# Performance work log

Hardware: AMD Instinct MI355X
Metric: run time of the kernel (lower is better)

The kernel has to match this reference:

```python
import jax, jax.numpy as jnp
import numpy as np

B, T, E, H, HD, L, V = 4, 1024, 1024, 16, 64, 8, 32000
FF = 4 * E
SCALE = E ** -0.5  # NOTE: original scales by embed_size**-0.5, not head_size**-0.5
EPS = 1e-5


def setup_inputs() -> dict:
    key = jax.random.key(0)
    ks = jax.random.split(key, 22)
    s = 0.02
    n = lambda k, shape: (jax.random.normal(k, shape) * s).astype(jnp.float32)
    return {
        "x": jax.random.randint(ks[0], (B, T), 0, V),
        "tok_emb": n(ks[1], (V, E)),
        "pos_emb": n(ks[2], (T, E)),
        "Wq": n(ks[3], (L, H, E, HD)),
        "Wk": n(ks[4], (L, H, E, HD)),
        "Wv": n(ks[5], (L, H, E, HD)),
        "Wproj": n(ks[6], (L, E, E)),
        "bproj": jnp.zeros((L, E), jnp.float32),
        "ln1g": jnp.ones((L, E), jnp.float32),
        "ln1b": jnp.zeros((L, E), jnp.float32),
        "ln2g": jnp.ones((L, E), jnp.float32),
        "ln2b": jnp.zeros((L, E), jnp.float32),
        "W1": n(ks[7], (L, E, FF)),
        "b1": jnp.zeros((L, FF), jnp.float32),
        "W2": n(ks[8], (L, FF, E)),
        "b2": jnp.zeros((L, E), jnp.float32),
        "lnfg": jnp.ones((E,), jnp.float32),
        "lnfb": jnp.zeros((E,), jnp.float32),
        "Wout": n(ks[9], (E, V)),
        "bout": jnp.zeros((V,), jnp.float32),
    }


def _ln(x, g, b):
    m = jnp.mean(x, axis=-1, keepdims=True)
    v = jnp.mean(jnp.square(x - m), axis=-1, keepdims=True)
    return (x - m) * jax.lax.rsqrt(v + EPS) * g + b


def _gpt(x, tok_emb, pos_emb, Wq, Wk, Wv, Wproj, bproj, ln1g, ln1b, ln2g, ln2b,
         W1, b1, W2, b2, lnfg, lnfb, Wout, bout):
    h = tok_emb[x] + pos_emb[None, :, :]  # [B,T,E]
    mask = jnp.tril(jnp.ones((T, T), bool))  # causal

    def block(h, p):
        wq, wk, wv, wp, bp, g1, bb1n, g2, bb2n, w1, bb1, w2, bb2 = p
        xn = _ln(h, g1, bb1n)
        q = jnp.einsum('bte,hed->bhtd', xn, wq)
        k = jnp.einsum('bte,hed->bhtd', xn, wk)
        v = jnp.einsum('bte,hed->bhtd', xn, wv)
        scores = jnp.einsum('bhtd,bhsd->bhts', q, k) * SCALE
        scores = jnp.where(mask, scores, -jnp.inf)
        w = jax.nn.softmax(scores, axis=-1)
        a = jnp.einsum('bhts,bhsd->bhtd', w, v)  # [B,H,T,HD]
        a = a.transpose(0, 2, 1, 3).reshape(B, T, E)  # concat heads
        h = h + jnp.einsum('bte,ef->btf', a, wp) + bp
        xn2 = _ln(h, g2, bb2n)
        ff = jax.nn.gelu(jnp.einsum('bte,ef->btf', xn2, w1) + bb1, approximate=False)
        h = h + jnp.einsum('btf,fe->bte', ff, w2) + bb2
        return h, None

    params = (Wq, Wk, Wv, Wproj, bproj, ln1g, ln1b, ln2g, ln2b, W1, b1, W2, b2)
    h, _ = jax.lax.scan(block, h, params)
    h = _ln(h, lnfg, lnfb)
    return jnp.einsum('bte,ev->btv', h, Wout) + bout  # logits [B,T,V]


def reference(x, tok_emb, pos_emb, Wq, Wk, Wv, Wproj, bproj, ln1g, ln1b, ln2g,
              ln2b, W1, b1, W2, b2, lnfg, lnfb, Wout, bout):
    return _gpt(x, tok_emb, pos_emb, Wq, Wk, Wv, Wproj, bproj, ln1g, ln1b,
                ln2g, ln2b, W1, b1, W2, b2, lnfg, lnfb, Wout, bout)
```

## Files before the change

kernel.cpp:

```cpp
#include <hip/hip_runtime.h>

#define B_ 4
#define T_ 1024
#define E_ 1024
#define H_ 16
#define HD_ 64
#define L_ 8
#define V_ 32000
#define FF_ 4096
#define M_ (B_*T_)

typedef unsigned short u16;
typedef __attribute__((ext_vector_type(8))) short bf16x8;
typedef __attribute__((ext_vector_type(4))) float f32x4;

#define AS1V(p) ((__attribute__((address_space(1))) void*)(p))
#define AS3V(p) ((__attribute__((address_space(3))) void*)(p))
#define XSW(row) (((row) & 7) << 4)

#define GBAR  asm volatile("s_barrier" ::: "memory")
#define WVM8  asm volatile("s_waitcnt vmcnt(8)" ::: "memory")
#define WVM0  asm volatile("s_waitcnt vmcnt(0)" ::: "memory")

__device__ __forceinline__ u16 f2bf(float f) {
    unsigned int u = __float_as_uint(f);
    u += 0x7FFFu + ((u >> 16) & 1u);
    return (u16)(u >> 16);
}
__device__ __forceinline__ float bf2f(u16 v) {
    return __uint_as_float(((unsigned int)v) << 16);
}
__device__ __forceinline__ float ldf(const float* p, long i) { return p[i]; }
__device__ __forceinline__ float ldf(const u16*   p, long i) { return bf2f(p[i]); }

__device__ __forceinline__ int xcd_swz(int orig, int nwg) {
    int q8 = nwg >> 3, r8 = nwg & 7;
    int xcd = orig & 7, sub = orig >> 3;
    return (xcd < r8 ? xcd*(q8+1) : r8*(q8+1) + (xcd-r8)*q8) + sub;
}

template<typename ST>
__global__ void k_transpose(const ST* __restrict__ src, u16* __restrict__ dst,
                            int K, int N, long srs, long drs,
                            int ZH, long szb, long szh, long dzb, long dzh)
{
    __shared__ float tile[32][33];
    int z = blockIdx.z; int zb = z / ZH, zh = z % ZH;
    const ST* s = src + (long)zb*szb + (long)zh*szh;
    u16* d = dst + (long)zb*dzb + (long)zh*dzh;
    int k0 = blockIdx.y * 32, n0 = blockIdx.x * 32;
    int tx = threadIdx.x, ty = threadIdx.y;
    for (int i = ty; i < 32; i += 8) {
        int k = k0 + i, n = n0 + tx;
        tile[i][tx] = (k < K && n < N) ? ldf(s, (long)k*srs + n) : 0.f;
    }
    __syncthreads();
    for (int i = ty; i < 32; i += 8) {
        int n = n0 + i, k = k0 + tx;
        if (n < N && k < K) d[(long)n*drs + k] = f2bf(tile[tx][i]);
    }
}

__global__ void k_embed(const int* __restrict__ x, const float* __restrict__ tok,
                        const float* __restrict__ pos, float* __restrict__ h)
{
    long i = (long)blockIdx.x * 256 + threadIdx.x;
    int e4 = (int)(i & (E_/4 - 1));
    long bt = i >> 8;
    int t = (int)(bt & (T_ - 1));
    int id = x[bt];
    float4 a = *(const float4*)(tok + (long)id*E_ + e4*4);
    float4 p = *(const float4*)(pos + (long)t*E_ + e4*4);
    float4 o; o.x=a.x+p.x; o.y=a.y+p.y; o.z=a.z+p.z; o.w=a.w+p.w;
    *(float4*)(h + bt*E_ + e4*4) = o;
}

__global__ void k_ln(const float* __restrict__ in, const float* __restrict__ g,
                     const float* __restrict__ b, u16* __restrict__ out)
{
    int row = blockIdx.x, tid = threadIdx.x;
    float4 v = *(const float4*)(in + (long)row*E_ + tid*4);
    float s = v.x + v.y + v.z + v.w;
    float ss = v.x*v.x + v.y*v.y + v.z*v.z + v.w*v.w;
    #pragma unroll
    for (int o = 32; o; o >>= 1) { s += __shfl_down(s, o); ss += __shfl_down(ss, o); }
    __shared__ float r0[4], r1[4];
    if ((tid & 63) == 0) { r0[tid >> 6] = s; r1[tid >> 6] = ss; }
    __syncthreads();
    s  = r0[0] + r0[1] + r0[2] + r0[3];
    ss = r1[0] + r1[1] + r1[2] + r1[3];
    float mean = s * (1.f/E_);
    float rstd = rsqrtf(ss * (1.f/E_) - mean*mean + 1e-5f);
    float4 gv = *(const float4*)(g + tid*4);
    float4 bv = *(const float4*)(b + tid*4);
    ushort4 pk;
    pk.x = f2bf((v.x - mean)*rstd*gv.x + bv.x);
    pk.y = f2bf((v.y - mean)*rstd*gv.y + bv.y);
    pk.z = f2bf((v.z - mean)*rstd*gv.z + bv.z);
    pk.w = f2bf((v.w - mean)*rstd*gv.w + bv.w);
    *(ushort4*)(out + (long)row*E_ + tid*4) = pk;
}

__global__ __launch_bounds__(256, 2)
void k_flash(const u16* __restrict__ qkv, const u16* __restrict__ vt,
             u16* __restrict__ attno)
{
    __shared__ alignas(16) char lds[65536];
    const int wg = xcd_swz(blockIdx.x, gridDim.x);
    const int bh = wg >> 3, qt = 7 - (wg & 7);
    const int b = bh >> 4, hh = bh & 15;

    const int tid = threadIdx.x, w = tid >> 6, lane = tid & 63;
    const int fr = lane & 15, sel = lane >> 4;
    const int xs = XSW(fr);

    const char* qb = (const char*)(qkv + (long)b*T_*3*E_ + (size_t)hh*HD_);
    const char* kb = (const char*)(qkv + (long)b*T_*3*E_ + E_ + (size_t)hh*HD_);
    const char* vb = (const char*)(vt + (size_t)bh*HD_*T_);
    const int q0 = qt << 7;

    bf16x8 qa[2][2];
    #pragma unroll
    for (int rf = 0; rf < 2; ++rf)
        #pragma unroll
        for (int t = 0; t < 2; ++t) {
            int row = q0 + w*32 + rf*16 + fr;
            qa[rf][t] = *(const bf16x8*)(qb + (long)row*(3*E_*2) + t*64 + sel*16);
        }

    f32x4 oacc[2][4];
    float mrow[2][4], lrow[2][4];
    #pragma unroll
    for (int rf = 0; rf < 2; ++rf) {
        #pragma unroll
        for (int cf = 0; cf < 4; ++cf) oacc[rf][cf] = (f32x4){0.f,0.f,0.f,0.f};
        #pragma unroll
        for (int r = 0; r < 4; ++r) { mrow[rf][r] = -1e30f; lrow[rf][r] = 0.f; }
    }

    char* Ks  = lds;
    char* Vts = lds + 16384;
    char* Pw  = lds + 32768 + w*8192;

    for (int kv = 0; kv <= qt; ++kv) {
        const int s0 = kv << 7;
        __syncthreads();
        #pragma unroll
        for (int c = 0; c < 4; ++c) {
            int o = c*4096 + tid*16;
            int row = o >> 7;
            int offl = (o & 127) ^ XSW(row);
            const char* ga = kb + (long)(s0 + row)*(3*E_*2) + offl;
            __builtin_amdgcn_global_load_lds(AS1V(ga), AS3V(Ks + c*4096 + (tid >> 6)*1024), 16, 0, 0);
        }
        #pragma unroll
        for (int c = 0; c < 4; ++c) {
            int o = c*4096 + tid*16;
            int row = o >> 8;
            int offl = (o & 255) ^ XSW(row);
            const char* ga = vb + (long)row*(T_*2) + s0*2 + offl;
            __builtin_amdgcn_global_load_lds(AS1V(ga), AS3V(Vts + c*4096 + (tid >> 6)*1024), 16, 0, 0);
        }
        __syncthreads();

        f32x4 sacc[2][8];
        #pragma unroll
        for (int rf = 0; rf < 2; ++rf)
            #pragma unroll
            for (int cf = 0; cf < 8; ++cf) sacc[rf][cf] = (f32x4){0.f,0.f,0.f,0.f};
        __builtin_amdgcn_s_setprio(1);
        #pragma unroll
        for (int t = 0; t < 2; ++t) {
            bf16x8 kf[8];
            #pragma unroll
            for (int cf = 0; cf < 8; ++cf) {
                int srow = cf*16 + fr;
                kf[cf] = *(const bf16x8*)(Ks + srow*128 + ((t*64 + sel*16) ^ xs));
            }
            #pragma unroll
            for (int rf = 0; rf < 2; ++rf)
                #pragma unroll
                for (int cf = 0; cf < 8; ++cf)
                    sacc[rf][cf] = __builtin_amdgcn_mfma_f32_16x16x32_bf16(
                        qa[rf][t], kf[cf], sacc[rf][cf], 0, 0, 0);
        }
        __builtin_amdgcn_s_setprio(0);

        const bool diag = (kv == qt);
        #pragma unroll
        for (int rf = 0; rf < 2; ++rf)
            #pragma unroll
            for (int r = 0; r < 4; ++r) {
                int rowg = q0 + w*32 + rf*16 + sel*4 + r;
                float mx = -1e30f;
                #pragma unroll
                for (int cf = 0; cf < 8; ++cf) {
                    float v = sacc[rf][cf][r] * 0.03125f;
                    if (diag && (s0 + cf*16 + fr) > rowg) v = -1e30f;
                    sacc[rf][cf][r] = v;
                    mx = fmaxf(mx, v);
                }
                #pragma unroll
                for (int o = 1; o < 16; o <<= 1) mx = fmaxf(mx, __shfl_xor(mx, o));
                float mold = mrow[rf][r];
                float mnew = fmaxf(mold, mx);
                float alpha = __expf(mold - mnew);
                float sum = 0.f;
                #pragma unroll
                for (int cf = 0; cf < 8; ++cf) {
                    float p = __expf(sacc[rf][cf][r] - mnew);
                    sacc[rf][cf][r] = p;
                    sum += p;
                }
                #pragma unroll
                for (int o = 1; o < 16; o <<= 1) sum += __shfl_xor(sum, o);
                mrow[rf][r] = mnew;
                lrow[rf][r] = lrow[rf][r]*alpha + sum;
                #pragma unroll
                for (int cf = 0; cf < 4; ++cf) oacc[rf][cf][r] *= alpha;
            }

        #pragma unroll
        for (int rf = 0; rf < 2; ++rf)
            #pragma unroll
            for (int r = 0; r < 4; ++r) {
                int rl = rf*16 + sel*4 + r;
                char* base = Pw + rl*256;
                int sw = XSW(rl);
                #pragma unroll
                for (int cf = 0; cf < 8; ++cf)
                    *(u16*)(base + ((cf*32 + fr*2) ^ sw)) = f2bf(sacc[rf][cf][r]);
            }

        __builtin_amdgcn_s_setprio(1);
        #pragma unroll
        for (int ts = 0; ts < 4; ++ts) {
            bf16x8 pa[2], vf[4];
            #pragma unroll
            for (int rf = 0; rf < 2; ++rf)
                pa[rf] = *(const bf16x8*)(Pw + (rf*16 + fr)*256 + ((ts*64 + sel*16) ^ xs));
            #pragma unroll
            for (int cf = 0; cf < 4; ++cf)
                vf[cf] = *(const bf16x8*)(Vts + (cf*16 + fr)*256 + ((ts*64 + sel*16) ^ xs));
            #pragma unroll
            for (int rf = 0; rf < 2; ++rf)
                #pragma unroll
                for (int cf = 0; cf < 4; ++cf)
                    oacc[rf][cf] = __builtin_amdgcn_mfma_f32_16x16x32_bf16(
                        pa[rf], vf[cf], oacc[rf][cf], 0, 0, 0);
        }
        __builtin_amdgcn_s_setprio(0);
    }

    u16* ab = attno + ((long)b*T_ + q0 + w*32)*E_ + (size_t)hh*HD_;
    #pragma unroll
    for (int rf = 0; rf < 2; ++rf)
        #pragma unroll
        for (int r = 0; r < 4; ++r) {
            float rinv = 1.f / lrow[rf][r];
            int rl = rf*16 + sel*4 + r;
            #pragma unroll
            for (int cf = 0; cf < 4; ++cf)
                ab[(long)rl*E_ + cf*16 + fr] = f2bf(oacc[rf][cf][r] * rinv);
        }
}

__global__ __launch_bounds__(256, 2)
void k_gemm128(const u16* __restrict__ A, const u16* __restrict__ Bt,
               float* __restrict__ C, const float* __restrict__ bias,
               const float* __restrict__ res,
               long lda, long ldb, long ldc, int Kk, int nTN)
{
    __shared__ alignas(128) char lds[65536];
    const int wg = xcd_swz(blockIdx.x, gridDim.x);
    const int m0 = (wg / nTN) << 7, n0 = (wg % nTN) << 7;

    const int tid = threadIdx.x, wid = tid >> 6, lane = tid & 63;
    const int fr = lane & 15, sel = lane >> 4;
    const int wr = wid >> 1, wc = wid & 1;
    const int xs = XSW(fr);
    const int KT = Kk >> 6;

    const long lda2 = lda*2, ldb2 = ldb*2;
    const int rowL = tid >> 3;
    const int offl = (((tid & 7) ^ (rowL & 7)) << 4);
    const char* pA = (const char*)A + ((long)(m0 + rowL))*lda2 + offl;
    const char* pB = (const char*)Bt + ((long)(n0 + rowL))*ldb2 + offl;
    char* ldwA = lds + (wid << 10);
    char* ldwB = lds + 32768 + (wid << 10);

    auto stageA = [&](int kt) {
        const int d = (kt & 1) << 14;
        const long kb = (long)kt << 7;
        #pragma unroll
        for (int c = 0; c < 4; ++c)
            __builtin_amdgcn_global_load_lds(AS1V(pA + (long)(c << 5)*lda2 + kb),
                                             AS3V(ldwA + d + (c << 12)), 16, 0, 0);
    };
    auto stageB = [&](int kt) {
        const int d = (kt & 1) << 14;
        const long kb = (long)kt << 7;
        #pragma unroll
        for (int c = 0; c < 4; ++c)
            __builtin_amdgcn_global_load_lds(AS1V(pB + (long)(c << 5)*ldb2 + kb),
                                             AS3V(ldwB + d + (c << 12)), 16, 0, 0);
    };

    f32x4 acc[4][4];
    #pragma unroll
    for (int i = 0; i < 4; ++i)
        #pragma unroll
        for (int j = 0; j < 4; ++j) acc[i][j] = (f32x4){0.f,0.f,0.f,0.f};

    stageA(0); stageB(0); stageA(1); stageB(1);
    WVM8; GBAR;

    for (int t = 0; t < KT; ++t) {
        const int d = (t & 1) << 14;
        bf16x8 a[4][2], b[4][2];
        #pragma unroll
        for (int m = 0; m < 4; ++m)
            #pragma unroll
            for (int tt = 0; tt < 2; ++tt)
                a[m][tt] = *(const bf16x8*)(lds + d +
                    (((wr*64 + m*16 + fr) << 7) + ((sel*16 + tt*64) ^ xs)));
        #pragma unroll
        for (int n = 0; n < 4; ++n)
            #pragma unroll
            for (int tt = 0; tt < 2; ++tt)
                b[n][tt] = *(const bf16x8*)(lds + 32768 + d +
                    (((wc*64 + n*16 + fr) << 7) + ((sel*16 + tt*64) ^ xs)));
        __builtin_amdgcn_s_setprio(1);
        #pragma unroll
        for (int m = 0; m < 4; ++m)
            #pragma unroll
            for (int n = 0; n < 4; ++n)
                #pragma unroll
                for (int tt = 0; tt < 2; ++tt)
                    acc[m][n] = __builtin_amdgcn_mfma_f32_16x16x32_bf16(
                        a[m][tt], b[n][tt], acc[m][n], 0, 0, 0);
        __builtin_amdgcn_s_setprio(0);
        GBAR;
        if (t + 2 < KT) {
            stageA(t+2); stageB(t+2);
            WVM8;
        } else {
            WVM0;
        }
        GBAR;
    }

    #pragma unroll
    for (int m = 0; m < 4; ++m) {
        #pragma unroll
        for (int rr = 0; rr < 4; ++rr) {
            const int row = m0 + wr*64 + m*16 + sel*4 + rr;
            #pragma unroll
            for (int n = 0; n < 4; ++n) {
                const int col = n0 + wc*64 + n*16 + fr;
                long idx = (long)row*ldc + col;
                C[idx] = acc[m][n][rr] + bias[col] + res[idx];
            }
        }
    }
}

template<int MODE>
__global__ __launch_bounds__(512, 2)
void k_gemm256(const u16* __restrict__ A, const u16* __restrict__ Bt,
               void* __restrict__ Cv, const float* __restrict__ bias,
               long lda, long ldb, long ldc, int Kk, int nTN)
{
    __shared__ alignas(128) char lds[131072];
    const int wg = xcd_swz(blockIdx.x, gridDim.x);
    const int m0 = (wg / nTN) << 8, n0 = (wg % nTN) << 8;

    const int tid = threadIdx.x, wid = tid >> 6, lane = tid & 63;
    const int fr = lane & 15, sel = lane >> 4;
    const int wr = wid >> 2, wc = wid & 3;
    const int xs = XSW(fr);
    const int KT = Kk >> 6;

    const long lda2 = lda*2, ldb2 = ldb*2;
    const int rowL = tid >> 3;
    const int offl = (((tid & 7) ^ (rowL & 7)) << 4);
    const char* pA = (const char*)A + ((long)(m0 + rowL))*lda2 + offl;
    const char* pB = (const char*)Bt + ((long)(n0 + rowL))*ldb2 + offl;
    char* ldwA = lds + (wid << 10);
    char* ldwB = lds + 65536 + (wid << 10);

    auto stageA = [&](int kt) {
        const int d = (kt & 1) << 15;
        const long kb = (long)kt << 7;
        #pragma unroll
        for (int hq = 0; hq < 4; ++hq)
            __builtin_amdgcn_global_load_lds(AS1V(pA + (long)(hq << 6)*lda2 + kb),
                                             AS3V(ldwA + d + (hq << 13)), 16, 0, 0);
    };
    auto stageB = [&](int kt) {
        const int d = (kt & 1) << 15;
        const long kb = (long)kt << 7;
        #pragma unroll
        for (int hq = 0; hq < 4; ++hq)
            __builtin_amdgcn_global_load_lds(AS1V(pB + (long)(hq << 6)*ldb2 + kb),
                                             AS3V(ldwB + d + (hq << 13)), 16, 0, 0);
    };

    bf16x8 a[4][2], b[2][2][2];
    f32x4 acc[8][4];
    #pragma unroll
    for (int i = 0; i < 8; ++i)
        #pragma unroll
        for (int j = 0; j < 4; ++j) acc[i][j] = (f32x4){0.f,0.f,0.f,0.f};

    auto readA = [&](int d, int rh) {
        const int base = (d << 15) + ((wr*128 + rh*64 + fr) << 7) + (sel << 4);
        #pragma unroll
        for (int rf = 0; rf < 4; ++rf)
            #pragma unroll
            for (int t = 0; t < 2; ++t)
                a[rf][t] = *(const bf16x8*)(lds + ((base + (rf << 11) + (t << 6)) ^ xs));
    };
    auto readB = [&](int d, int ch) {
        const int base = 65536 + (d << 15) + ((wc*64 + ch*32 + fr) << 7) + (sel << 4);
        #pragma unroll
        for (int cf = 0; cf < 2; ++cf)
            #pragma unroll
            for (int t = 0; t < 2; ++t)
                b[ch][cf][t] = *(const bf16x8*)(lds + ((base + (cf << 11) + (t << 6)) ^ xs));
    };
    auto mfma16 = [&](int rh, int ch) {
        __builtin_amdgcn_s_setprio(1);
        #pragma unroll
        for (int rf = 0; rf < 4; ++rf)
            #pragma unroll
            for (int cf = 0; cf < 2; ++cf)
                #pragma unroll
                for (int t = 0; t < 2; ++t)
                    acc[rh*4+rf][ch*2+cf] = __builtin_amdgcn_mfma_f32_16x16x32_bf16(
                        a[rf][t], b[ch][cf][t], acc[rh*4+rf][ch*2+cf], 0, 0, 0);
        __builtin_amdgcn_s_setprio(0);
    };

    stageA(0); stageB(0); stageA(1); stageB(1);
    WVM8; GBAR;

    for (int kt = 0; kt < KT; kt += 2) {
        const bool pf = (kt + 2) < KT;
        readA(0,0); readB(0,0);
        GBAR; mfma16(0,0); GBAR;
        readB(0,1);
        GBAR; mfma16(0,1); GBAR;
        readA(0,1); if (pf) stageB(kt+2);
        GBAR; mfma16(1,1); GBAR;
        if (pf) stageA(kt+2);
        GBAR; mfma16(1,0);
        if (pf) { WVM8; } else { WVM0; }
        GBAR;
        readA(1,0); readB(1,0);
        GBAR; mfma16(0,0); GBAR;
        readB(1,1);
        GBAR; mfma16(0,1); GBAR;
        readA(1,1); if (pf) stageB(kt+3);
        GBAR; mfma16(1,1); GBAR;
        if (pf) stageA(kt+3);
        GBAR; mfma16(1,0);
        if (pf) { WVM8; }
        GBAR;
    }

    #pragma unroll
    for (int rf = 0; rf < 8; ++rf) {
        const int row0 = m0 + wr*128 + rf*16 + (sel << 2);
        #pragma unroll
        for (int rr = 0; rr < 4; ++rr) {
            const long rbase = (long)(row0 + rr) * ldc;
            #pragma unroll
            for (int cf = 0; cf < 4; ++cf) {
                const int col = n0 + wc*64 + cf*16 + fr;
                float v = acc[rf][cf][rr];
                if constexpr (MODE == 0) {
                    ((u16*)Cv)[rbase + col] = f2bf(v);
                } else if constexpr (MODE == 2) {
                    float tt = v + bias[col];
                    ((u16*)Cv)[rbase + col] = f2bf(tt * 0.5f * (1.f + erff(tt * 0.70710678118f)));
                } else {
                    ((float*)Cv)[rbase + col] = v + bias[col];
                }
            }
        }
    }
}

extern "C" void kernel_launch(void* const* d_in, const int* in_sizes, int n_in,
                              void* d_out, int out_size, void* d_ws, size_t ws_size,
                              hipStream_t stream)
{
    (void)in_sizes; (void)n_in; (void)out_size; (void)ws_size;
    const int*   x   = (const int*)  d_in[0];
    const float* tok = (const float*)d_in[1];
    const float* pos = (const float*)d_in[2];
    const float* Wq  = (const float*)d_in[3];
    const float* Wk  = (const float*)d_in[4];
    const float* Wv  = (const float*)d_in[5];
    const float* Wp  = (const float*)d_in[6];
    const float* bp  = (const float*)d_in[7];
    const float* g1  = (const float*)d_in[8];
    const float* bb1 = (const float*)d_in[9];
    const float* g2  = (const float*)d_in[10];
    const float* bb2 = (const float*)d_in[11];
    const float* W1  = (const float*)d_in[12];
    const float* b1  = (const float*)d_in[13];
    const float* W2  = (const float*)d_in[14];
    const float* b2  = (const float*)d_in[15];
    const float* gF  = (const float*)d_in[16];
    const float* bF  = (const float*)d_in[17];
    const float* Wo  = (const float*)d_in[18];
    const float* bo  = (const float*)d_in[19];
    float* out = (float*)d_out;

    char* wsp = (char*)d_ws;
    auto alloc = [&](size_t bytes) { char* p = wsp; wsp += (bytes + 255) & ~(size_t)255; return p; };
    u16* WqkvT  = (u16*)alloc((size_t)L_*3*E_*E_*2);
    u16* WprojT = (u16*)alloc((size_t)L_*E_*E_*2);
    u16* W1T    = (u16*)alloc((size_t)L_*FF_*E_*2);
    u16* W2T    = (u16*)alloc((size_t)L_*E_*FF_*2);
    u16* WoutT  = (u16*)alloc((size_t)V_*E_*2);
    float* h    = (float*)alloc((size_t)M_*E_*4);
    u16* xn     = (u16*)alloc((size_t)M_*E_*2);
    u16* qkv    = (u16*)alloc((size_t)M_*3*E_*2);
    u16* vt     = (u16*)alloc((size_t)B_*H_*HD_*T_*2);
    u16* attno  = (u16*)alloc((size_t)M_*E_*2);
    u16* ffb    = (u16*)alloc((size_t)M_*FF_*2);

    dim3 tb(32, 8);
    k_transpose<float><<<dim3(HD_/32, E_/32, L_*H_), tb, 0, stream>>>(
        Wq, WqkvT, E_, HD_, (long)HD_, (long)E_,
        H_, (long)H_*E_*HD_, (long)E_*HD_, (long)3*E_*E_, (long)HD_*E_);
    k_transpose<float><<<dim3(HD_/32, E_/32, L_*H_), tb, 0, stream>>>(
        Wk, WqkvT + (size_t)E_*E_, E_, HD_, (long)HD_, (long)E_,
        H_, (long)H_*E_*HD_, (long)E_*HD_, (long)3*E_*E_, (long)HD_*E_);
    k_transpose<float><<<dim3(HD_/32, E_/32, L_*H_), tb, 0, stream>>>(
        Wv, WqkvT + (size_t)2*E_*E_, E_, HD_, (long)HD_, (long)E_,
        H_, (long)H_*E_*HD_, (long)E_*HD_, (long)3*E_*E_, (long)HD_*E_);
    k_transpose<float><<<dim3(E_/32, E_/32, L_), tb, 0, stream>>>(
        Wp, WprojT, E_, E_, (long)E_, (long)E_, 1, (long)E_*E_, 0, (long)E_*E_, 0);
    k_transpose<float><<<dim3(FF_/32, E_/32, L_), tb, 0, stream>>>(
        W1, W1T, E_, FF_, (long)FF_, (long)E_, 1, (long)E_*FF_, 0, (long)FF_*E_, 0);
    k_transpose<float><<<dim3(E_/32, FF_/32, L_), tb, 0, stream>>>(
        W2, W2T, FF_, E_, (long)E_, (long)FF_, 1, (long)FF_*E_, 0, (long)E_*FF_, 0);
    k_transpose<float><<<dim3(V_/32, E_/32, 1), tb, 0, stream>>>(
        Wo, WoutT, E_, V_, (long)V_, (long)E_, 1, 0, 0, 0, 0);
    k_embed<<<dim3(M_*E_/4/256), dim3(256), 0, stream>>>(x, tok, pos, h);

    auto gemm256 = [&](int mode, const u16* A, const u16* Bt, void* C, const float* bias,
                       int Mm, int Nn, int Kk, long lda, long ldb, long ldc) {
        int nTN = Nn >> 8;
        dim3 g((Mm >> 8) * nTN), blk(512);
        switch (mode) {
        case 0: k_gemm256<0><<<g, blk, 0, stream>>>(A, Bt, C, bias, lda, ldb, ldc, Kk, nTN); break;
        case 2: k_gemm256<2><<<g, blk, 0, stream>>>(A, Bt, C, bias, lda, ldb, ldc, Kk, nTN); break;
        case 4: k_gemm256<4><<<g, blk, 0, stream>>>(A, Bt, C, bias, lda, ldb, ldc, Kk, nTN); break;
        }
    };

    for (int l = 0; l < L_; ++l) {
        k_ln<<<dim3(M_), dim3(256), 0, stream>>>(h, g1 + (size_t)l*E_, bb1 + (size_t)l*E_, xn);
        gemm256(0, xn, WqkvT + (size_t)l*3*E_*E_, qkv, nullptr,
                M_, 3*E_, E_, (long)E_, (long)E_, (long)3*E_);
        k_transpose<u16><<<dim3(HD_/32, T_/32, B_*H_), tb, 0, stream>>>(
            qkv + 2*E_, vt, T_, HD_, (long)3*E_, (long)T_,
            H_, (long)T_*3*E_, (long)HD_, (long)H_*HD_*T_, (long)HD_*T_);
        k_flash<<<dim3(B_*H_*8), dim3(256), 0, stream>>>(qkv, vt, attno);
        k_gemm128<<<dim3((M_/128)*(E_/128)), dim3(256), 0, stream>>>(
            attno, WprojT + (size_t)l*E_*E_, h, bp + (size_t)l*E_, h,
            (long)E_, (long)E_, (long)E_, E_, E_/128);
        k_ln<<<dim3(M_), dim3(256), 0, stream>>>(h, g2 + (size_t)l*E_, bb2 + (size_t)l*E_, xn);
        gemm256(2, xn, W1T + (size_t)l*FF_*E_, ffb, b1 + (size_t)l*FF_,
                M_, FF_, E_, (long)E_, (long)E_, (long)FF_);
        k_gemm128<<<dim3((M_/128)*(E_/128)), dim3(256), 0, stream>>>(
            ffb, W2T + (size_t)l*E_*FF_, h, b2 + (size_t)l*E_, h,
            (long)FF_, (long)FF_, (long)E_, FF_, E_/128);
    }
    k_ln<<<dim3(M_), dim3(256), 0, stream>>>(h, gF, bF, xn);
    gemm256(4, xn, WoutT, out, bo, M_, V_, E_, (long)E_, (long)E_, (long)V_);
}
```

Before: 3.308 ms.

## Restage 256-tile GEMM in half-tile chunks and switch to M-major tile order

The 256x256 GEMM's global-to-LDS staging is split into half-tile chunks, issued right after each LDS fragment read. An `lgkmcnt(0)` wait before each barrier makes it safe to overwrite a buffer half as soon as it has been consumed. The aim is to spread memory traffic more evenly across the MFMA phases, using a `vmcnt(4)` wait and clamped K indices so the wait count stays uniform. Both GEMM kernels also now walk tiles M-fastest instead of N-fastest, which changes which A and B tiles are in the cache at the same time. The extra waits and redundant clamped loads at the end of the K loop add some overhead and barrier pressure.

```diff
diff --git a/kernel.cpp b/kernel.cpp
--- a/kernel.cpp
+++ b/kernel.cpp
@@ -19,6 +19,8 @@
 #define XSW(row) (((row) & 7) << 4)
 
 #define GBAR  asm volatile("s_barrier" ::: "memory")
+#define WLG0  asm volatile("s_waitcnt lgkmcnt(0)" ::: "memory")
+#define WVM4  asm volatile("s_waitcnt vmcnt(4)" ::: "memory")
 #define WVM8  asm volatile("s_waitcnt vmcnt(8)" ::: "memory")
 #define WVM0  asm volatile("s_waitcnt vmcnt(0)" ::: "memory")
 
@@ -269,11 +271,11 @@
 void k_gemm128(const u16* __restrict__ A, const u16* __restrict__ Bt,
                float* __restrict__ C, const float* __restrict__ bias,
                const float* __restrict__ res,
-               long lda, long ldb, long ldc, int Kk, int nTN)
+               long lda, long ldb, long ldc, int Kk, int nTM)
 {
     __shared__ alignas(128) char lds[65536];
     const int wg = xcd_swz(blockIdx.x, gridDim.x);
-    const int m0 = (wg / nTN) << 7, n0 = (wg % nTN) << 7;
+    const int m0 = (wg % nTM) << 7, n0 = (wg / nTM) << 7;
 
     const int tid = threadIdx.x, wid = tid >> 6, lane = tid & 63;
     const int fr = lane & 15, sel = lane >> 4;
@@ -369,11 +371,11 @@
 __global__ __launch_bounds__(512, 2)
 void k_gemm256(const u16* __restrict__ A, const u16* __restrict__ Bt,
                void* __restrict__ Cv, const float* __restrict__ bias,
-               long lda, long ldb, long ldc, int Kk, int nTN)
+               long lda, long ldb, long ldc, int Kk, int nTM)
 {
     __shared__ alignas(128) char lds[131072];
     const int wg = xcd_swz(blockIdx.x, gridDim.x);
-    const int m0 = (wg / nTN) << 8, n0 = (wg % nTN) << 8;
+    const int m0 = (wg % nTM) << 8, n0 = (wg / nTM) << 8;
 
     const int tid = threadIdx.x, wid = tid >> 6, lane = tid & 63;
     const int fr = lane & 15, sel = lane >> 4;
@@ -381,29 +383,25 @@
     const int xs = XSW(fr);
     const int KT = Kk >> 6;
 
-    const long lda2 = lda*2, ldb2 = ldb*2;
-    const int rowL = tid >> 3;
-    const int offl = (((tid & 7) ^ (rowL & 7)) << 4);
-    const char* pA = (const char*)A + ((long)(m0 + rowL))*lda2 + offl;
-    const char* pB = (const char*)Bt + ((long)(n0 + rowL))*ldb2 + offl;
-    char* ldwA = lds + (wid << 10);
-    char* ldwB = lds + 65536 + (wid << 10);
-
-    auto stageA = [&](int kt) {
-        const int d = (kt & 1) << 15;
-        const long kb = (long)kt << 7;
-        #pragma unroll
-        for (int hq = 0; hq < 4; ++hq)
-            __builtin_amdgcn_global_load_lds(AS1V(pA + (long)(hq << 6)*lda2 + kb),
-                                             AS3V(ldwA + d + (hq << 13)), 16, 0, 0);
-    };
-    auto stageB = [&](int kt) {
-        const int d = (kt & 1) << 15;
-        const long kb = (long)kt << 7;
-        #pragma unroll
-        for (int hq = 0; hq < 4; ++hq)
-            __builtin_amdgcn_global_load_lds(AS1V(pB + (long)(hq << 6)*ldb2 + kb),
-                                             AS3V(ldwB + d + (hq << 13)), 16, 0, 0);
+    const char* Asrc = (const char*)A + (long)m0 * lda * 2;
+    const char* Bsrc = (const char*)Bt + (long)n0 * ldb * 2;
+
+    auto stage = [&](int mat, int h, int kt) {
+        const int d = kt & 1;
+        const int kc = kt < KT ? kt : KT - 1;
+        const char* src = mat ? Bsrc : Asrc;
+        const long ldd = (mat ? ldb : lda) * 2;
+        const long kbyte = (long)kc << 7;
+        const int mo = mat << 16;
+        #pragma unroll
+        for (int q = 0; q < 2; ++q) {
+            const int o = (h << 14) + (q << 13) + tid*16;
+            const int row = o >> 7;
+            const int offl = (o & 127) ^ XSW(row);
+            const char* ga = src + (long)row*ldd + kbyte + offl;
+            char* ldst = lds + mo + (d << 15) + (h << 14) + (q << 13) + (wid << 10);
+            __builtin_amdgcn_global_load_lds(AS1V(ga), AS3V(ldst), 16, 0, 0);
+        }
     };
 
     bf16x8 a[4][2], b[2][2][2];
@@ -442,31 +440,27 @@
         __builtin_amdgcn_s_setprio(0);
     };
 
-    stageA(0); stageB(0); stageA(1); stageB(1);
-    WVM8; GBAR;
+    stage(0,0,0); stage(0,1,0); stage(1,0,0); stage(1,1,0);
+    stage(0,0,1); stage(0,1,1); stage(1,0,1); stage(1,1,1);
+    WVM4; GBAR;
 
     for (int kt = 0; kt < KT; kt += 2) {
-        const bool pf = (kt + 2) < KT;
-        readA(0,0); readB(0,0);
-        GBAR; mfma16(0,0); GBAR;
-        readB(0,1);
-        GBAR; mfma16(0,1); GBAR;
-        readA(0,1); if (pf) stageB(kt+2);
-        GBAR; mfma16(1,1); GBAR;
-        if (pf) stageA(kt+2);
-        GBAR; mfma16(1,0);
-        if (pf) { WVM8; } else { WVM0; }
-        GBAR;
-        readA(1,0); readB(1,0);
-        GBAR; mfma16(0,0); GBAR;
-        readB(1,1);
-        GBAR; mfma16(0,1); GBAR;
-        readA(1,1); if (pf) stageB(kt+3);
-        GBAR; mfma16(1,1); GBAR;
-        if (pf) stageA(kt+3);
-        GBAR; mfma16(1,0);
-        if (pf) { WVM8; }
-        GBAR;
+        readA(0,0); readB(0,0); stage(0,0,kt+1);
+        GBAR; mfma16(0,0); WLG0; GBAR;
+        readB(0,1); stage(0,1,kt+1);
+        GBAR; mfma16(0,1); WLG0; GBAR;
+        readA(0,1); stage(1,0,kt+2);
+        GBAR; mfma16(1,1); WLG0; GBAR;
+        stage(1,1,kt+2);
+        GBAR; mfma16(1,0); WLG0; WVM4; GBAR;
+        readA(1,0); readB(1,0); stage(0,0,kt+2);
+        GBAR; mfma16(0,0); WLG0; GBAR;
+        readB(1,1); stage(0,1,kt+2);
+        GBAR; mfma16(0,1); WLG0; GBAR;
+        readA(1,1); stage(1,0,kt+3);
+        GBAR; mfma16(1,1); WLG0; GBAR;
+        stage(1,1,kt+3);
+        GBAR; mfma16(1,0); WLG0; WVM4; GBAR;
     }
 
     #pragma unroll
@@ -555,12 +549,12 @@
 
     auto gemm256 = [&](int mode, const u16* A, const u16* Bt, void* C, const float* bias,
                        int Mm, int Nn, int Kk, long lda, long ldb, long ldc) {
-        int nTN = Nn >> 8;
-        dim3 g((Mm >> 8) * nTN), blk(512);
+        int nTM = Mm >> 8;
+        dim3 g(nTM * (Nn >> 8)), blk(512);
         switch (mode) {
-        case 0: k_gemm256<0><<<g, blk, 0, stream>>>(A, Bt, C, bias, lda, ldb, ldc, Kk, nTN); break;
-        case 2: k_gemm256<2><<<g, blk, 0, stream>>>(A, Bt, C, bias, lda, ldb, ldc, Kk, nTN); break;
-        case 4: k_gemm256<4><<<g, blk, 0, stream>>>(A, Bt, C, bias, lda, ldb, ldc, Kk, nTN); break;
+        case 0: k_gemm256<0><<<g, blk, 0, stream>>>(A, Bt, C, bias, lda, ldb, ldc, Kk, nTM); break;
+        case 2: k_gemm256<2><<<g, blk, 0, stream>>>(A, Bt, C, bias, lda, ldb, ldc, Kk, nTM); break;
+        case 4: k_gemm256<4><<<g, blk, 0, stream>>>(A, Bt, C, bias, lda, ldb, ldc, Kk, nTM); break;
         }
     };
 
@@ -574,13 +568,13 @@
         k_flash<<<dim3(B_*H_*8), dim3(256), 0, stream>>>(qkv, vt, attno);
         k_gemm128<<<dim3((M_/128)*(E_/128)), dim3(256), 0, stream>>>(
             attno, WprojT + (size_t)l*E_*E_, h, bp + (size_t)l*E_, h,
-            (long)E_, (long)E_, (long)E_, E_, E_/128);
+            (long)E_, (long)E_, (long)E_, E_, M_/128);
         k_ln<<<dim3(M_), dim3(256), 0, stream>>>(h, g2 + (size_t)l*E_, bb2 + (size_t)l*E_, xn);
         gemm256(2, xn, W1T + (size_t)l*FF_*E_, ffb, b1 + (size_t)l*FF_,
                 M_, FF_, E_, (long)E_, (long)E_, (long)FF_);
         k_gemm128<<<dim3((M_/128)*(E_/128)), dim3(256), 0, stream>>>(
             ffb, W2T + (size_t)l*E_*FF_, h, b2 + (size_t)l*E_, h,
-            (long)FF_, (long)FF_, (long)E_, FF_, E_/128);
+            (long)FF_, (long)FF_, (long)E_, FF_, M_/128);
     }
     k_ln<<<dim3(M_), dim3(256), 0, stream>>>(h, gF, bF, xn);
     gemm256(4, xn, WoutT, out, bo, M_, V_, E_, (long)E_, (long)E_, (long)V_);
```

After: 2.874 ms, median of 2. -13.1%, faster.
